# Kernel optimization log

Hardware: AMD Instinct MI355X
Metric: run time of the kernel (lower is better)

## Reference

```python
import jax, jax.numpy as jnp
import numpy as np

C = 4          # in_channels: number of TT objects in the input list
B = 4096       # batch_size
OUT = 32       # out_channels
ROWS = 17408   # in_channels * num_parameter = 4 * 4352


def setup_inputs() -> dict:
    key = jax.random.key(0)
    k1, k2, k3, k4 = jax.random.split(key, 4)
    cores_first = jax.random.normal(k1, (C, 128, B), dtype=jnp.float32)        # first core per TT object, flattened
    cores_mid = jax.random.normal(k2, (C, 2, 2048, B), dtype=jnp.float32)      # two middle cores per object
    cores_last = jax.random.normal(k3, (C, 128, B), dtype=jnp.float32)         # last core per object
    weight = jax.random.normal(k4, (ROWS, OUT), dtype=jnp.float32) * (1.0 / np.sqrt(ROWS))
    return {"cores_first": cores_first, "cores_mid": cores_mid,
            "cores_last": cores_last, "weight": weight}


def reference(cores_first, cores_mid, cores_last, weight):
    # Faithful to the torch loop: for each TT object, copy core0, core1, core2, core3
    # (each flattened to (-1, B)) into consecutive row blocks of buffer I, then GEMM.
    c, _, b = cores_first.shape
    # per-object row block in loop order: [first | mid0 | mid1 | last] -> (C, 4352, B)
    I = jnp.concatenate(
        [cores_first, cores_mid.reshape(c, -1, b), cores_last], axis=1
    ).reshape(-1, b)  # (ROWS, B)
    return jnp.einsum('io,ib->bo', weight, I)  # (B, OUT)
```

## Files before the change

### kernel.cpp

```cpp
#include <hip/hip_runtime.h>


#define BATCH   4096
#define OUTC    32
#define NCHUNK  68
#define BPC     2
#define BTILES  8

__global__ __launch_bounds__(256) void cwl_partial(
    const float* __restrict__ cf,
    const float* __restrict__ cm,
    const float* __restrict__ cl,
    const float* __restrict__ w,
    float* __restrict__ ws)
{
    __shared__ float wlds[BPC * 128 * OUTC];

    const int chunk = blockIdx.x % NCHUNK;
    const int btile = blockIdx.x / NCHUNK;
    const int tid   = threadIdx.x;
    const int wv    = tid >> 6;
    const int lane  = tid & 63;
    const int ohalf = wv & 1;
    const int bsub  = wv >> 1;
    const int b0    = btile * 512 + bsub * 256 + lane * 4;

    {
        float4* wl = (float4*)wlds;
#pragma unroll
        for (int h = 0; h < BPC; ++h) {
            const int m = chunk * BPC + h;
            const float4* wg = (const float4*)(w + (size_t)m * 128 * OUTC);
#pragma unroll
            for (int k = 0; k < 4; ++k)
                wl[h * 1024 + k * 256 + tid] = wg[k * 256 + tid];
        }
    }
    __syncthreads();

    float acc[16][4];
#pragma unroll
    for (int o = 0; o < 16; ++o)
#pragma unroll
        for (int bi = 0; bi < 4; ++bi) acc[o][bi] = 0.0f;

    for (int h = 0; h < BPC; ++h) {
        const int m = chunk * BPC + h;
        const int c = m / 34;
        const int j = m - c * 34;
        const float* src = (j == 0)  ? cf + (size_t)c * 128 * BATCH
                         : (j == 33) ? cl + (size_t)c * 128 * BATCH
                         : cm + ((size_t)c * 4096 + (size_t)(j - 1) * 128) * BATCH;
        const float4* xp  = (const float4*)src + (b0 >> 2);
        const float*  wlh = wlds + h * 128 * OUTC;

        for (int r0 = 0; r0 < 128; r0 += 4) {
            float4 x[4];
#pragma unroll
            for (int u = 0; u < 4; ++u)
                x[u] = xp[(size_t)(r0 + u) * (BATCH / 4)];
#pragma unroll
            for (int u = 0; u < 4; ++u) {
                const float4* wr = (const float4*)(wlh + (r0 + u) * OUTC + ohalf * 16);
#pragma unroll
                for (int q = 0; q < 4; ++q) {
                    const float4 wq = wr[q];
#pragma unroll
                    for (int jj = 0; jj < 4; ++jj) {
                        const float wj = ((const float*)&wq)[jj];
                        const int o = q * 4 + jj;
                        acc[o][0] = fmaf(x[u].x, wj, acc[o][0]);
                        acc[o][1] = fmaf(x[u].y, wj, acc[o][1]);
                        acc[o][2] = fmaf(x[u].z, wj, acc[o][2]);
                        acc[o][3] = fmaf(x[u].w, wj, acc[o][3]);
                    }
                }
            }
        }
    }

#pragma unroll
    for (int bi = 0; bi < 4; ++bi) {
        float4* dst = (float4*)(ws + ((size_t)chunk * BATCH + (b0 + bi)) * OUTC
                                + ohalf * 16);
#pragma unroll
        for (int q = 0; q < 4; ++q)
            dst[q] = make_float4(acc[q*4+0][bi], acc[q*4+1][bi],
                                 acc[q*4+2][bi], acc[q*4+3][bi]);
    }
}

__global__ __launch_bounds__(256) void cwl_reduce(
    const float* __restrict__ ws, float* __restrict__ out)
{
    const int t = blockIdx.x * 256 + threadIdx.x;
    float s = 0.0f;
#pragma unroll
    for (int c = 0; c < NCHUNK; ++c)
        s += ws[(size_t)c * (BATCH * OUTC) + t];
    out[t] = s;
}

extern "C" void kernel_launch(void* const* d_in, const int* in_sizes, int n_in,
                              void* d_out, int out_size, void* d_ws, size_t ws_size,
                              hipStream_t stream)
{
    const float* cf = (const float*)d_in[0];
    const float* cm = (const float*)d_in[1];
    const float* cl = (const float*)d_in[2];
    const float* w  = (const float*)d_in[3];
    float* out = (float*)d_out;
    float* ws  = (float*)d_ws;

    cwl_partial<<<dim3(NCHUNK * BTILES), dim3(256), 0, stream>>>(cf, cm, cl, w, ws);
    cwl_reduce<<<dim3((BATCH * OUTC) / 256), dim3(256), 0, stream>>>(ws, out);
}
```

Measured before the change: 467.7 us.

## Split work into one block per row chunk and double-buffer input loads

Each block now handles a single 128-row chunk instead of two, doubling the grid to raise parallelism across CUs, and adds an occupancy hint to launch_bounds. The inner loop double-buffers the global float4 loads of the input rows in registers, so the next four rows are in flight while the current four are multiplied. The reduce kernel uses four independent accumulators for more memory-level parallelism. In exchange, the workspace of partial sums doubles, adding write and read traffic, and the larger register footprint may fight the occupancy target.

```diff
diff --git a/kernel.cpp b/kernel.cpp
--- a/kernel.cpp
+++ b/kernel.cpp
@@ -3,18 +3,17 @@
 
 #define BATCH   4096
 #define OUTC    32
-#define NCHUNK  68
-#define BPC     2
+#define NCHUNK  136
 #define BTILES  8
 
-__global__ __launch_bounds__(256) void cwl_partial(
+__global__ __launch_bounds__(256, 4) void cwl_partial(
     const float* __restrict__ cf,
     const float* __restrict__ cm,
     const float* __restrict__ cl,
     const float* __restrict__ w,
     float* __restrict__ ws)
 {
-    __shared__ float wlds[BPC * 128 * OUTC];
+    __shared__ float wlds[128 * OUTC];
 
     const int chunk = blockIdx.x % NCHUNK;
     const int btile = blockIdx.x / NCHUNK;
@@ -26,16 +25,25 @@
     const int b0    = btile * 512 + bsub * 256 + lane * 4;
 
     {
+        const float4* wg = (const float4*)(w + (size_t)chunk * 128 * OUTC);
         float4* wl = (float4*)wlds;
 #pragma unroll
-        for (int h = 0; h < BPC; ++h) {
-            const int m = chunk * BPC + h;
-            const float4* wg = (const float4*)(w + (size_t)m * 128 * OUTC);
+        for (int k = 0; k < 4; ++k)
+            wl[k * 256 + tid] = wg[k * 256 + tid];
+    }
+
+    const int c = chunk / 34;
+    const int j = chunk % 34;
+    const float* src = (j == 0)  ? cf + (size_t)c * 128 * BATCH
+                     : (j == 33) ? cl + (size_t)c * 128 * BATCH
+                     : cm + ((size_t)c * 4096 + (size_t)(j - 1) * 128) * BATCH;
+    const float4* xp = (const float4*)src + (b0 >> 2);
+
+    float4 xa[4], xb[4];
 #pragma unroll
-            for (int k = 0; k < 4; ++k)
-                wl[h * 1024 + k * 256 + tid] = wg[k * 256 + tid];
-        }
-    }
+    for (int u = 0; u < 4; ++u)
+        xa[u] = xp[(size_t)u * (BATCH / 4)];
+
     __syncthreads();
 
     float acc[16][4];
@@ -44,39 +52,39 @@
 #pragma unroll
         for (int bi = 0; bi < 4; ++bi) acc[o][bi] = 0.0f;
 
-    for (int h = 0; h < BPC; ++h) {
-        const int m = chunk * BPC + h;
-        const int c = m / 34;
-        const int j = m - c * 34;
-        const float* src = (j == 0)  ? cf + (size_t)c * 128 * BATCH
-                         : (j == 33) ? cl + (size_t)c * 128 * BATCH
-                         : cm + ((size_t)c * 4096 + (size_t)(j - 1) * 128) * BATCH;
-        const float4* xp  = (const float4*)src + (b0 >> 2);
-        const float*  wlh = wlds + h * 128 * OUTC;
+    const float* wlh = wlds + ohalf * 16;
 
-        for (int r0 = 0; r0 < 128; r0 += 4) {
-            float4 x[4];
+#define CWL_COMPUTE(XREG, RBASE)                                          \
+    do {                                                                  \
+        _Pragma("unroll")                                                 \
+        for (int u = 0; u < 4; ++u) {                                     \
+            const float4* wr = (const float4*)(wlh + (RBASE + u) * OUTC); \
+            _Pragma("unroll")                                             \
+            for (int q = 0; q < 4; ++q) {                                 \
+                const float4 wq = wr[q];      \
+                _Pragma("unroll")                                         \
+                for (int jj = 0; jj < 4; ++jj) {                          \
+                    const float wj = ((const float*)&wq)[jj];             \
+                    const int o = q * 4 + jj;                             \
+                    acc[o][0] = fmaf(XREG[u].x, wj, acc[o][0]);           \
+                    acc[o][1] = fmaf(XREG[u].y, wj, acc[o][1]);           \
+                    acc[o][2] = fmaf(XREG[u].z, wj, acc[o][2]);           \
+                    acc[o][3] = fmaf(XREG[u].w, wj, acc[o][3]);           \
+                }                                                         \
+            }                                                             \
+        }                                                                 \
+    } while (0)
+
+    for (int r0 = 0; r0 < 128; r0 += 8) {
 #pragma unroll
-            for (int u = 0; u < 4; ++u)
-                x[u] = xp[(size_t)(r0 + u) * (BATCH / 4)];
+        for (int u = 0; u < 4; ++u)
+            xb[u] = xp[(size_t)(r0 + 4 + u) * (BATCH / 4)];
+        CWL_COMPUTE(xa, r0);
+        const int rn = (r0 + 8 < 128) ? r0 + 8 : 124;
 #pragma unroll
-            for (int u = 0; u < 4; ++u) {
-                const float4* wr = (const float4*)(wlh + (r0 + u) * OUTC + ohalf * 16);
-#pragma unroll
-                for (int q = 0; q < 4; ++q) {
-                    const float4 wq = wr[q];
-#pragma unroll
-                    for (int jj = 0; jj < 4; ++jj) {
-                        const float wj = ((const float*)&wq)[jj];
-                        const int o = q * 4 + jj;
-                        acc[o][0] = fmaf(x[u].x, wj, acc[o][0]);
-                        acc[o][1] = fmaf(x[u].y, wj, acc[o][1]);
-                        acc[o][2] = fmaf(x[u].z, wj, acc[o][2]);
-                        acc[o][3] = fmaf(x[u].w, wj, acc[o][3]);
-                    }
-                }
-            }
-        }
+        for (int u = 0; u < 4; ++u)
+            xa[u] = xp[(size_t)(rn + u) * (BATCH / 4)];
+        CWL_COMPUTE(xb, r0 + 4);
     }
 
 #pragma unroll
@@ -94,11 +102,15 @@
     const float* __restrict__ ws, float* __restrict__ out)
 {
     const int t = blockIdx.x * 256 + threadIdx.x;
-    float s = 0.0f;
-#pragma unroll
-    for (int c = 0; c < NCHUNK; ++c)
-        s += ws[(size_t)c * (BATCH * OUTC) + t];
-    out[t] = s;
+    float s0 = 0.f, s1 = 0.f, s2 = 0.f, s3 = 0.f;
+#pragma unroll 4
+    for (int c = 0; c < NCHUNK; c += 4) {
+        s0 += ws[(size_t)(c+0) * (BATCH * OUTC) + t];
+        s1 += ws[(size_t)(c+1) * (BATCH * OUTC) + t];
+        s2 += ws[(size_t)(c+2) * (BATCH * OUTC) + t];
+        s3 += ws[(size_t)(c+3) * (BATCH * OUTC) + t];
+    }
+    out[t] = (s0 + s1) + (s2 + s3);
 }
 
 extern "C" void kernel_launch(void* const* d_in, const int* in_sizes, int n_in,
```

Result: faster. 436.8 us (-6.6%).

## Stream activations through double-buffered LDS via async global_load_lds and split chunks finer

Applied to the files above, without the earlier changes.

Each block now handles one 128-row chunk instead of two, which doubles the grid and the number of partial slices. Activation rows and weights are copied into LDS with global_load_lds DMA, and activations use a double-buffered 8-row stage pipeline so the next stage's loads overlap the current stage's FMAs. The reduce kernel uses four independent accumulators to add ILP. In exchange, the partial workspace and reduce traffic both double, and a barrier is added per stage.

```diff
diff --git a/kernel.cpp b/kernel.cpp
--- a/kernel.cpp
+++ b/kernel.cpp
@@ -1,20 +1,29 @@
 #include <hip/hip_runtime.h>
+#include <stdint.h>
 
 
-#define BATCH   4096
-#define OUTC    32
-#define NCHUNK  68
-#define BPC     2
-#define BTILES  8
+#define BATCH  4096
+#define OUTC   32
+#define NCHUNK 136
+#define BTILES 8
+#define RSTAGE 8
+#define NSTAGE 16
 
-__global__ __launch_bounds__(256) void cwl_partial(
+__device__ __forceinline__ void dma16(const float* g, float* l) {
+    __builtin_amdgcn_global_load_lds(
+        (const __attribute__((address_space(1))) void*)g,
+        (__attribute__((address_space(3))) void*)l, 16, 0, 0);
+}
+
+__global__ __launch_bounds__(256, 3) void cwl_partial(
     const float* __restrict__ cf,
     const float* __restrict__ cm,
     const float* __restrict__ cl,
     const float* __restrict__ w,
     float* __restrict__ ws)
 {
-    __shared__ float wlds[BPC * 128 * OUTC];
+    __shared__ float wlds[128 * OUTC];
+    __shared__ float xlds[2][RSTAGE * 512];
 
     const int chunk = blockIdx.x % NCHUNK;
     const int btile = blockIdx.x / NCHUNK;
@@ -23,18 +32,26 @@
     const int lane  = tid & 63;
     const int ohalf = wv & 1;
     const int bsub  = wv >> 1;
-    const int b0    = btile * 512 + bsub * 256 + lane * 4;
 
-    {
-        float4* wl = (float4*)wlds;
+    const int c = chunk / 34;
+    const int j = chunk % 34;
+    const float* src = (j == 0)  ? cf + (size_t)c * 128 * BATCH
+                     : (j == 33) ? cl + (size_t)c * 128 * BATCH
+                     : cm + ((size_t)c * 4096 + (size_t)(j - 1) * 128) * BATCH;
+    const float* srcg = src + btile * 512;
+    const float* wg   = w + (size_t)chunk * 128 * OUTC;
+
 #pragma unroll
-        for (int h = 0; h < BPC; ++h) {
-            const int m = chunk * BPC + h;
-            const float4* wg = (const float4*)(w + (size_t)m * 128 * OUTC);
+    for (int t = 0; t < 4; ++t) {
+        const int seg = wv * 4 + t;
+        dma16(wg + seg * 256 + lane * 4, wlds + seg * 256);
+    }
 #pragma unroll
-            for (int k = 0; k < 4; ++k)
-                wl[h * 1024 + k * 256 + tid] = wg[k * 256 + tid];
-        }
+    for (int t = 0; t < 4; ++t) {
+        const int row  = wv * 2 + (t >> 1);
+        const int half = t & 1;
+        dma16(srcg + (size_t)row * BATCH + half * 256 + lane * 4,
+              &xlds[0][row * 512 + half * 256]);
     }
     __syncthreads();
 
@@ -44,41 +61,44 @@
 #pragma unroll
         for (int bi = 0; bi < 4; ++bi) acc[o][bi] = 0.0f;
 
-    for (int h = 0; h < BPC; ++h) {
-        const int m = chunk * BPC + h;
-        const int c = m / 34;
-        const int j = m - c * 34;
-        const float* src = (j == 0)  ? cf + (size_t)c * 128 * BATCH
-                         : (j == 33) ? cl + (size_t)c * 128 * BATCH
-                         : cm + ((size_t)c * 4096 + (size_t)(j - 1) * 128) * BATCH;
-        const float4* xp  = (const float4*)src + (b0 >> 2);
-        const float*  wlh = wlds + h * 128 * OUTC;
+    const int xoff = bsub * 256 + lane * 4;
 
-        for (int r0 = 0; r0 < 128; r0 += 4) {
-            float4 x[4];
+    for (int s = 0; s < NSTAGE; ++s) {
+        if (s + 1 < NSTAGE) {
+            float* xn = xlds[(s + 1) & 1];
+            const int r0 = (s + 1) * RSTAGE;
 #pragma unroll
-            for (int u = 0; u < 4; ++u)
-                x[u] = xp[(size_t)(r0 + u) * (BATCH / 4)];
+            for (int t = 0; t < 4; ++t) {
+                const int row  = wv * 2 + (t >> 1);
+                const int half = t & 1;
+                dma16(srcg + (size_t)(r0 + row) * BATCH + half * 256 + lane * 4,
+                      xn + row * 512 + half * 256);
+            }
+        }
+        const float* xb   = xlds[s & 1];
+        const float* wrow = wlds + s * RSTAGE * OUTC + ohalf * 16;
 #pragma unroll
-            for (int u = 0; u < 4; ++u) {
-                const float4* wr = (const float4*)(wlh + (r0 + u) * OUTC + ohalf * 16);
+        for (int r = 0; r < RSTAGE; ++r) {
+            const float4 x = *(const float4*)(xb + r * 512 + xoff);
+            const float4* wr = (const float4*)(wrow + r * OUTC);
 #pragma unroll
-                for (int q = 0; q < 4; ++q) {
-                    const float4 wq = wr[q];
+            for (int q = 0; q < 4; ++q) {
+                const float4 wq = wr[q];
 #pragma unroll
-                    for (int jj = 0; jj < 4; ++jj) {
-                        const float wj = ((const float*)&wq)[jj];
-                        const int o = q * 4 + jj;
-                        acc[o][0] = fmaf(x[u].x, wj, acc[o][0]);
-                        acc[o][1] = fmaf(x[u].y, wj, acc[o][1]);
-                        acc[o][2] = fmaf(x[u].z, wj, acc[o][2]);
-                        acc[o][3] = fmaf(x[u].w, wj, acc[o][3]);
-                    }
+                for (int jj = 0; jj < 4; ++jj) {
+                    const float wj = ((const float*)&wq)[jj];
+                    const int o = q * 4 + jj;
+                    acc[o][0] = fmaf(x.x, wj, acc[o][0]);
+                    acc[o][1] = fmaf(x.y, wj, acc[o][1]);
+                    acc[o][2] = fmaf(x.z, wj, acc[o][2]);
+                    acc[o][3] = fmaf(x.w, wj, acc[o][3]);
                 }
             }
         }
+        __syncthreads();
     }
 
+    const int b0 = btile * 512 + bsub * 256 + lane * 4;
 #pragma unroll
     for (int bi = 0; bi < 4; ++bi) {
         float4* dst = (float4*)(ws + ((size_t)chunk * BATCH + (b0 + bi)) * OUTC
@@ -94,11 +114,15 @@
     const float* __restrict__ ws, float* __restrict__ out)
 {
     const int t = blockIdx.x * 256 + threadIdx.x;
-    float s = 0.0f;
-#pragma unroll
-    for (int c = 0; c < NCHUNK; ++c)
-        s += ws[(size_t)c * (BATCH * OUTC) + t];
-    out[t] = s;
+    float s0 = 0.f, s1 = 0.f, s2 = 0.f, s3 = 0.f;
+#pragma unroll 4
+    for (int c = 0; c < NCHUNK; c += 4) {
+        s0 += ws[(size_t)(c+0) * (BATCH * OUTC) + t];
+        s1 += ws[(size_t)(c+1) * (BATCH * OUTC) + t];
+        s2 += ws[(size_t)(c+2) * (BATCH * OUTC) + t];
+        s3 += ws[(size_t)(c+3) * (BATCH * OUTC) + t];
+    }
+    out[t] = (s0 + s1) + (s2 + s3);
 }
 
 extern "C" void kernel_launch(void* const* d_in, const int* in_sizes, int n_in,
```

Result: faster. 406.5 us (-13.1%).
